# Kernel tuning notes

Measured on AMD Instinct MI355X. Metric: run time of the kernel, lower is better.

The kernel has to match this reference:

```python
import jax, jax.numpy as jnp
import numpy as np

B, S, D, H = 4, 2048, 512, 8
HD = D // H  # 64


def setup_inputs() -> dict:
    key = jax.random.key(0)
    ks = jax.random.split(key, 7)
    scale = 1.0 / np.sqrt(D)
    return {
        "query": jax.random.normal(ks[0], (B, S, D), jnp.float32),
        "key": jax.random.normal(ks[1], (B, S, D), jnp.float32),
        "value": jax.random.normal(ks[2], (B, S, D), jnp.float32),
        # Only the `query` Linear and fc_out are actually used in the original forward
        "Wq": jax.random.uniform(ks[3], (D, D), jnp.float32, -scale, scale),
        "bq": jnp.zeros((D,), jnp.float32),
        "Wo": jax.random.uniform(ks[4], (D, D), jnp.float32, -scale, scale),
        "bo": jnp.zeros((D,), jnp.float32),
    }


def reference(query, key, value, Wq, bq, Wo, bo):
    # Faithful to source: Q, K, V all use the *query* projection (bug preserved)
    def proj(x):
        # [B,S,D] -> [B,H,S,HD]
        y = x @ Wq + bq
        return y.reshape(B, S, H, HD).transpose(0, 2, 1, 3)

    Q, K, V = proj(query), proj(key), proj(value)
    scores = jnp.einsum("bhqd,bhkd->bhqk", Q, K) / jnp.sqrt(jnp.float32(HD))
    attn = jax.nn.softmax(scores, axis=-1)
    x = jnp.einsum("bhqk,bhkd->bhqd", attn, V)
    x = x.transpose(0, 2, 1, 3).reshape(B, S, D)
    return x @ Wo + bo
```

## Files before the change

kernel.cpp:

```cpp
#include <hip/hip_runtime.h>
#include <math.h>

#define B_ 4
#define S_ 2048
#define D_ 512
#define H_ 8
#define HD_ 64
#define SZ_ (B_ * S_ * D_)
#define WSZ_ (D_ * D_)
#define BSH_ (B_ * S_ * H_)

#define QSCALE_ 0.18033688011112042f

typedef _Float16 v4h __attribute__((ext_vector_type(4)));
typedef _Float16 v8h __attribute__((ext_vector_type(8)));
typedef float    v4f __attribute__((ext_vector_type(4)));

__device__ __forceinline__ void gload16(const void* g, void* l) {
    __builtin_amdgcn_global_load_lds((__attribute__((address_space(1))) void*)g,
                                     (__attribute__((address_space(3))) void*)l,
                                     16, 0, 0);
}

__device__ __forceinline__ v8h pack8(v4f a, v4f b) {
    return __builtin_shufflevector(__builtin_convertvector(a, v4h),
                                   __builtin_convertvector(b, v4h),
                                   0, 1, 2, 3, 4, 5, 6, 7);
}

__global__ __launch_bounds__(256) void wtrans_kernel(const float* __restrict__ Wq,
                                                     const float* __restrict__ Wo,
                                                     _Float16* __restrict__ Wt) {
    __shared__ float Ts[64][132];
    const int kc = blockIdx.x, nt = blockIdx.y, mat = blockIdx.z;
    const float* W = mat ? Wo : Wq;
    const int k0 = kc * 64, n0 = nt * 128;
    const int t = threadIdx.x;
#pragma unroll
    for (int i = 0; i < 8; i++) {
        int s2 = t + i * 256;
        int kk = s2 >> 5, nc = (s2 & 31) * 4;
        *(float4*)&Ts[kk][nc] = *(const float4*)&W[(size_t)(k0 + kk) * 512 + n0 + nc];
    }
    __syncthreads();
    _Float16* blk = Wt + (((size_t)mat * 4 + nt) * 8 + kc) * 8192;
#pragma unroll
    for (int i = 0; i < 4; i++) {
        int s2 = t + i * 256;
        int r = s2 >> 3, s = s2 & 7;
        int kl = (s ^ (r & 7)) * 8;
        v8h p;
#pragma unroll
        for (int j = 0; j < 8; j++) p[j] = (_Float16)Ts[kl + j][r];
        *(v8h*)&blk[r * 64 + s * 8] = p;
    }
}

__global__ __launch_bounds__(256) void convert_f16(const float* __restrict__ q,
                                                   const float* __restrict__ k,
                                                   const float* __restrict__ v,
                                                   _Float16* __restrict__ Xh) {
    const int kc = blockIdx.x, mt = blockIdx.y, z = blockIdx.z;
    const float* X = (z == 0) ? q : ((z == 1) ? k : v);
    _Float16* blk = Xh + (size_t)z * SZ_ + ((size_t)mt * 8 + kc) * 8192;
    const int t = threadIdx.x;
#pragma unroll
    for (int i = 0; i < 4; i++) {
        int s2 = t + i * 256;
        int r = s2 >> 3, s = s2 & 7;
        const float* src = X + (size_t)(mt * 128 + r) * 512 + kc * 64 + s * 8;
        *(v8h*)&blk[r * 64 + ((s ^ (r & 7)) * 8)] =
            pack8(*(const v4f*)src, *(const v4f*)(src + 4));
    }
}

__global__ __launch_bounds__(256) void combine_kernel(const float* __restrict__ Op,
                                                      const float* __restrict__ lp,
                                                      _Float16* __restrict__ Ah) {
    const int kc = blockIdx.x, mt = blockIdx.y;
    _Float16* blk = Ah + ((size_t)mt * 8 + kc) * 8192;
    const int t = threadIdx.x;
#pragma unroll
    for (int i = 0; i < 4; i++) {
        int s2 = t + i * 256;
        int r = s2 >> 3, s = s2 & 7;
        size_t row = (size_t)mt * 128 + r;
        const float* p = Op + row * 512 + kc * 64 + s * 8;
        const float* p2 = p + SZ_;
        float linv = __builtin_amdgcn_rcpf(lp[row * 8 + kc] + lp[BSH_ + row * 8 + kc]);
        v4f sa = (*(const v4f*)p + *(const v4f*)p2) * linv;
        v4f sb = (*(const v4f*)(p + 4) + *(const v4f*)(p2 + 4)) * linv;
        *(v8h*)&blk[r * 64 + ((s ^ (r & 7)) * 8)] = pack8(sa, sb);
    }
}

__global__ __launch_bounds__(256) void proj_mfma(const _Float16* __restrict__ Xh,
                                                 const _Float16* __restrict__ Wt,
                                                 const float* __restrict__ bq,
                                                 _Float16* __restrict__ Qh,
                                                 _Float16* __restrict__ Kh,
                                                 _Float16* __restrict__ VT) {
    __shared__ __align__(16) _Float16 As[8192];
    __shared__ __align__(16) _Float16 Bs[8192];
    const int nt = blockIdx.x, mt = blockIdx.y, z = blockIdx.z;
    const int n0 = nt * 128, m0 = mt * 128;
    const int t = threadIdx.x, lane = t & 63, w = t >> 6;
    const int wm = w >> 1, wn = w & 1;
    const int quad = lane >> 4, l16 = lane & 15;

    const _Float16* Ab = Xh + (size_t)z * SZ_ + ((size_t)mt * 8) * 8192 + w * 512 + lane * 8;
    const _Float16* Bb = Wt + ((size_t)nt * 8) * 8192 + w * 512 + lane * 8;
    _Float16* Ad = As + w * 512;
    _Float16* Bd = Bs + w * 512;

    v4f acc[4][4];
#pragma unroll
    for (int mi = 0; mi < 4; mi++)
#pragma unroll
        for (int ni = 0; ni < 4; ni++) acc[mi][ni] = (v4f)0.f;

    for (int kc = 0; kc < 8; ++kc) {
        __syncthreads();
#pragma unroll
        for (int i = 0; i < 4; i++) {
            gload16(Ab + kc * 8192 + i * 2048, Ad + i * 2048);
            gload16(Bb + kc * 8192 + i * 2048, Bd + i * 2048);
        }
        __syncthreads();

#pragma unroll
        for (int ks = 0; ks < 2; ++ks) {
            const int sxx = (ks * 32 + quad * 8) ^ ((l16 & 7) * 8);
            v8h af[4], bf[4];
#pragma unroll
            for (int mi = 0; mi < 4; mi++)
                af[mi] = *(const v8h*)&As[(wm * 64 + mi * 16 + l16) * 64 + sxx];
#pragma unroll
            for (int ni = 0; ni < 4; ni++)
                bf[ni] = *(const v8h*)&Bs[(wn * 64 + ni * 16 + l16) * 64 + sxx];
#pragma unroll
            for (int mi = 0; mi < 4; mi++)
#pragma unroll
                for (int ni = 0; ni < 4; ni++)
                    acc[mi][ni] = __builtin_amdgcn_mfma_f32_16x16x32_f16(af[mi], bf[ni], acc[mi][ni], 0, 0, 0);
        }
    }

    if (z < 2) {
        _Float16* Y = z ? Kh : Qh;
        const float sc = z ? 1.f : QSCALE_;
#pragma unroll
        for (int mi = 0; mi < 4; mi++) {
            int mb = m0 + wm * 64 + mi * 16 + quad * 4;
#pragma unroll
            for (int ni = 0; ni < 4; ni++) {
                int n = n0 + wn * 64 + ni * 16 + l16;
                float bj = bq[n];
#pragma unroll
                for (int r = 0; r < 4; r++)
                    Y[(size_t)(mb + r) * 512 + n] = (_Float16)((acc[mi][ni][r] + bj) * sc);
            }
        }
    } else {
#pragma unroll
        for (int mi = 0; mi < 4; mi++) {
            int tile0 = (m0 & 2047) + wm * 64;
            int pos = tile0 + (mi >> 1) * 32 + quad * 8 + (mi & 1) * 4;
            int b = m0 >> 11;
#pragma unroll
            for (int ni = 0; ni < 4; ni++) {
                int n = n0 + wn * 64 + ni * 16 + l16;
                int h = n >> 6, dd = n & 63;
                float bj = bq[n];
                v4h pk;
#pragma unroll
                for (int r = 0; r < 4; r++) pk[r] = (_Float16)(acc[mi][ni][r] + bj);
                *(v4h*)&VT[(((size_t)b * H_ + h) * HD_ + dd) * S_ + pos] = pk;
            }
        }
    }
}

__global__ __launch_bounds__(256) void outproj_mfma(const _Float16* __restrict__ Ah,
                                                    const _Float16* __restrict__ Wt,
                                                    const float* __restrict__ bo,
                                                    float* __restrict__ out) {
    __shared__ __align__(16) _Float16 As[8192];
    __shared__ __align__(16) _Float16 Bs[8192];
    const int nt = blockIdx.x, mt = blockIdx.y;
    const int n0 = nt * 128, m0 = mt * 128;
    const int t = threadIdx.x, lane = t & 63, w = t >> 6;
    const int wm = w >> 1, wn = w & 1;
    const int quad = lane >> 4, l16 = lane & 15;

    const _Float16* Ab = Ah + ((size_t)mt * 8) * 8192 + w * 512 + lane * 8;
    const _Float16* Bb = Wt + (size_t)(4 + nt) * 8 * 8192 + w * 512 + lane * 8;
    _Float16* Ad = As + w * 512;
    _Float16* Bd = Bs + w * 512;

    v4f acc[4][4];
#pragma unroll
    for (int mi = 0; mi < 4; mi++)
#pragma unroll
        for (int ni = 0; ni < 4; ni++) acc[mi][ni] = (v4f)0.f;

    for (int kc = 0; kc < 8; ++kc) {
        __syncthreads();
#pragma unroll
        for (int i = 0; i < 4; i++) {
            gload16(Ab + kc * 8192 + i * 2048, Ad + i * 2048);
            gload16(Bb + kc * 8192 + i * 2048, Bd + i * 2048);
        }
        __syncthreads();

#pragma unroll
        for (int ks = 0; ks < 2; ++ks) {
            const int sxx = (ks * 32 + quad * 8) ^ ((l16 & 7) * 8);
            v8h af[4], bf[4];
#pragma unroll
            for (int mi = 0; mi < 4; mi++)
                af[mi] = *(const v8h*)&As[(wm * 64 + mi * 16 + l16) * 64 + sxx];
#pragma unroll
            for (int ni = 0; ni < 4; ni++)
                bf[ni] = *(const v8h*)&Bs[(wn * 64 + ni * 16 + l16) * 64 + sxx];
#pragma unroll
            for (int mi = 0; mi < 4; mi++)
#pragma unroll
                for (int ni = 0; ni < 4; ni++)
                    acc[mi][ni] = __builtin_amdgcn_mfma_f32_16x16x32_f16(af[mi], bf[ni], acc[mi][ni], 0, 0, 0);
        }
    }

#pragma unroll
    for (int mi = 0; mi < 4; mi++) {
        int mb = m0 + wm * 64 + mi * 16 + quad * 4;
#pragma unroll
        for (int ni = 0; ni < 4; ni++) {
            int n = n0 + wn * 64 + ni * 16 + l16;
            float bj = bo[n];
#pragma unroll
            for (int r = 0; r < 4; r++)
                out[(size_t)(mb + r) * 512 + n] = acc[mi][ni][r] + bj;
        }
    }
}

__global__ __launch_bounds__(256) void flash_attn_f16(const _Float16* __restrict__ Qh,
                                                      const _Float16* __restrict__ Kh,
                                                      const _Float16* __restrict__ VT,
                                                      float* __restrict__ Op,
                                                      float* __restrict__ lp) {
    __shared__ _Float16 Ks[128 * 72];
    __shared__ _Float16 Vs[64 * 136];

    const int t     = threadIdx.x;
    const int lane  = t & 63;
    const int w     = t >> 6;
    const int quad  = lane >> 4;
    const int l16   = lane & 15;
    const int q0    = blockIdx.x * 128;
    const int h     = blockIdx.y;
    const int b     = blockIdx.z >> 1;
    const int split = blockIdx.z & 1;

    const size_t base  = (size_t)b * S_ * D_ + (size_t)h * HD_;
    const size_t vbase = ((size_t)b * H_ + h) * HD_ * (size_t)S_;

    v8h qf[2][2];
#pragma unroll
    for (int nb = 0; nb < 2; nb++) {
        const _Float16* qrow = Qh + base + (size_t)(q0 + w * 32 + nb * 16 + l16) * D_;
        qf[nb][0] = *(const v8h*)(qrow + quad * 8);
        qf[nb][1] = *(const v8h*)(qrow + 32 + quad * 8);
    }

    v4f o[2][4];
#pragma unroll
    for (int nb = 0; nb < 2; nb++)
#pragma unroll
        for (int i = 0; i < 4; i++) o[nb][i] = (v4f)0.f;
    float l_lane[2] = {0.f, 0.f};

    const int kbeg = split * (S_ / 2);
    const int kend = kbeg + S_ / 2;

    v8h kv[4], vv[4];
#define LOADKV(kk)                                                             \
    do {                                                                       \
        _Pragma("unroll") for (int i = 0; i < 4; i++) {                        \
            int c = t + i * 256;                                               \
            kv[i] = *(const v8h*)(Kh + base + (size_t)((kk) + (c >> 3)) * D_ + (c & 7) * 8); \
            vv[i] = *(const v8h*)(VT + vbase + (size_t)(c >> 4) * S_ + (kk) + (c & 15) * 8); \
        }                                                                      \
    } while (0)

    LOADKV(kbeg);

    for (int kk0 = kbeg; kk0 < kend; kk0 += 128) {
        __syncthreads();
#pragma unroll
        for (int i = 0; i < 4; i++) {
            int c = t + i * 256;
            *(v8h*)&Ks[(c >> 3) * 72 + (c & 7) * 8] = kv[i];
            *(v8h*)&Vs[(c >> 4) * 136 + (c & 15) * 8] = vv[i];
        }
        __syncthreads();

        if (kk0 + 128 < kend) LOADKV(kk0 + 128);

#pragma unroll
        for (int hh = 0; hh < 2; hh++) {
            v4f sc[4][2];
#pragma unroll
            for (int mb = 0; mb < 4; mb++)
#pragma unroll
                for (int nb = 0; nb < 2; nb++) sc[mb][nb] = (v4f)0.f;
#pragma unroll
            for (int ks = 0; ks < 2; ks++) {
#pragma unroll
                for (int mb = 0; mb < 4; mb++) {
                    v8h ak = *(const v8h*)&Ks[(hh * 64 + mb * 16 + l16) * 72 + ks * 32 + quad * 8];
#pragma unroll
                    for (int nb = 0; nb < 2; nb++)
                        sc[mb][nb] = __builtin_amdgcn_mfma_f32_16x16x32_f16(ak, qf[nb][ks], sc[mb][nb], 0, 0, 0);
                }
            }

            v4h pf[4][2];
#pragma unroll
            for (int nb = 0; nb < 2; nb++) {
#pragma unroll
                for (int mb = 0; mb < 4; mb++) {
                    v4f pv;
#pragma unroll
                    for (int r = 0; r < 4; r++) pv[r] = __builtin_amdgcn_exp2f(sc[mb][nb][r]);
                    pf[mb][nb] = __builtin_convertvector(pv, v4h);
                    l_lane[nb] += (pv[0] + pv[1]) + (pv[2] + pv[3]);
                }
            }

#pragma unroll
            for (int p = 0; p < 2; p++) {
#pragma unroll
                for (int dblk = 0; dblk < 4; dblk++) {
                    v8h vf2 = *(const v8h*)&Vs[(dblk * 16 + l16) * 136 + hh * 64 + p * 32 + quad * 8];
                    v4h vlo = __builtin_shufflevector(vf2, vf2, 0, 1, 2, 3);
                    v4h vhi = __builtin_shufflevector(vf2, vf2, 4, 5, 6, 7);
#pragma unroll
                    for (int nb = 0; nb < 2; nb++) {
                        o[nb][dblk] = __builtin_amdgcn_mfma_f32_16x16x16f16(vlo, pf[2 * p][nb], o[nb][dblk], 0, 0, 0);
                        o[nb][dblk] = __builtin_amdgcn_mfma_f32_16x16x16f16(vhi, pf[2 * p + 1][nb], o[nb][dblk], 0, 0, 0);
                    }
                }
            }
        }
    }
#undef LOADKV

    float* Ops = Op + (size_t)split * SZ_;
#pragma unroll
    for (int nb = 0; nb < 2; nb++) {
        float rs = l_lane[nb];
        rs += __shfl_xor(rs, 16);
        rs += __shfl_xor(rs, 32);
        int qrow = q0 + w * 32 + nb * 16 + l16;
        if (quad == 0)
            lp[(size_t)split * BSH_ + ((size_t)b * S_ + qrow) * H_ + h] = rs;
        const size_t rbase = base + (size_t)qrow * D_;
#pragma unroll
        for (int dblk = 0; dblk < 4; dblk++)
            *(v4f*)&Ops[rbase + dblk * 16 + quad * 4] = o[nb][dblk];
    }
}

extern "C" void kernel_launch(void* const* d_in, const int* in_sizes, int n_in,
                              void* d_out, int out_size, void* d_ws, size_t ws_size,
                              hipStream_t stream) {
    const float* query = (const float*)d_in[0];
    const float* key   = (const float*)d_in[1];
    const float* value = (const float*)d_in[2];
    const float* Wq    = (const float*)d_in[3];
    const float* bq    = (const float*)d_in[4];
    const float* Wo    = (const float*)d_in[5];
    const float* bo    = (const float*)d_in[6];
    float* out = (float*)d_out;

    _Float16* ws = (_Float16*)d_ws;
    _Float16* Qh = ws;
    _Float16* Kh = ws + (size_t)SZ_;
    _Float16* VT = ws + 2 * (size_t)SZ_;
    _Float16* Wt = ws + 3 * (size_t)SZ_;
    _Float16* Xh = ws + 3 * (size_t)SZ_ + 2 * (size_t)WSZ_;
    float*    Op = (float*)Xh;
    float*    lp = Op + 2 * (size_t)SZ_;
    _Float16* Ah = Qh;

    wtrans_kernel<<<dim3(8, 4, 2), 256, 0, stream>>>(Wq, Wo, Wt);
    convert_f16<<<dim3(8, 64, 3), 256, 0, stream>>>(query, key, value, Xh);
    proj_mfma<<<dim3(4, 64, 3), 256, 0, stream>>>(Xh, Wt, bq, Qh, Kh, VT);
    flash_attn_f16<<<dim3(S_ / 128, H_, B_ * 2), 256, 0, stream>>>(Qh, Kh, VT, Op, lp);
    combine_kernel<<<dim3(8, 64), 256, 0, stream>>>(Op, lp, Ah);
    outproj_mfma<<<dim3(4, 64), 256, 0, stream>>>(Ah, Wt, bo, out);
}
```

Before: 202.0 us.

## Drop KV split in attention, fuse normalization into epilogue, merge prep kernels

```diff
diff --git a/kernel.cpp b/kernel.cpp
--- a/kernel.cpp
+++ b/kernel.cpp
@@ -28,14 +28,33 @@
                                    0, 1, 2, 3, 4, 5, 6, 7);
 }
 
-__global__ __launch_bounds__(256) void wtrans_kernel(const float* __restrict__ Wq,
-                                                     const float* __restrict__ Wo,
-                                                     _Float16* __restrict__ Wt) {
+__global__ __launch_bounds__(256) void prep_f16(const float* __restrict__ q,
+                                                const float* __restrict__ k,
+                                                const float* __restrict__ v,
+                                                const float* __restrict__ Wq,
+                                                const float* __restrict__ Wo,
+                                                _Float16* __restrict__ Xh,
+                                                _Float16* __restrict__ Wt) {
+    const int kc = blockIdx.x, my = blockIdx.y, z = blockIdx.z;
+    const int t = threadIdx.x;
+    if (z < 3) {
+        const float* X = (z == 0) ? q : ((z == 1) ? k : v);
+        _Float16* blk = Xh + (size_t)z * SZ_ + ((size_t)my * 8 + kc) * 8192;
+#pragma unroll
+        for (int i = 0; i < 4; i++) {
+            int s2 = t + i * 256;
+            int r = s2 >> 3, s = s2 & 7;
+            const float* src = X + (size_t)(my * 128 + r) * 512 + kc * 64 + s * 8;
+            *(v8h*)&blk[r * 64 + ((s ^ (r & 7)) * 8)] =
+                pack8(*(const v4f*)src, *(const v4f*)(src + 4));
+        }
+        return;
+    }
+    if (my >= 8) return;
+    const int mat = my >> 2, nt = my & 3;
     __shared__ float Ts[64][132];
-    const int kc = blockIdx.x, nt = blockIdx.y, mat = blockIdx.z;
     const float* W = mat ? Wo : Wq;
     const int k0 = kc * 64, n0 = nt * 128;
-    const int t = threadIdx.x;
 #pragma unroll
     for (int i = 0; i < 8; i++) {
         int s2 = t + i * 256;
@@ -53,44 +72,6 @@
 #pragma unroll
         for (int j = 0; j < 8; j++) p[j] = (_Float16)Ts[kl + j][r];
         *(v8h*)&blk[r * 64 + s * 8] = p;
-    }
-}
-
-__global__ __launch_bounds__(256) void convert_f16(const float* __restrict__ q,
-                                                   const float* __restrict__ k,
-                                                   const float* __restrict__ v,
-                                                   _Float16* __restrict__ Xh) {
-    const int kc = blockIdx.x, mt = blockIdx.y, z = blockIdx.z;
-    const float* X = (z == 0) ? q : ((z == 1) ? k : v);
-    _Float16* blk = Xh + (size_t)z * SZ_ + ((size_t)mt * 8 + kc) * 8192;
-    const int t = threadIdx.x;
-#pragma unroll
-    for (int i = 0; i < 4; i++) {
-        int s2 = t + i * 256;
-        int r = s2 >> 3, s = s2 & 7;
-        const float* src = X + (size_t)(mt * 128 + r) * 512 + kc * 64 + s * 8;
-        *(v8h*)&blk[r * 64 + ((s ^ (r & 7)) * 8)] =
-            pack8(*(const v4f*)src, *(const v4f*)(src + 4));
-    }
-}
-
-__global__ __launch_bounds__(256) void combine_kernel(const float* __restrict__ Op,
-                                                      const float* __restrict__ lp,
-                                                      _Float16* __restrict__ Ah) {
-    const int kc = blockIdx.x, mt = blockIdx.y;
-    _Float16* blk = Ah + ((size_t)mt * 8 + kc) * 8192;
-    const int t = threadIdx.x;
-#pragma unroll
-    for (int i = 0; i < 4; i++) {
-        int s2 = t + i * 256;
-        int r = s2 >> 3, s = s2 & 7;
-        size_t row = (size_t)mt * 128 + r;
-        const float* p = Op + row * 512 + kc * 64 + s * 8;
-        const float* p2 = p + SZ_;
-        float linv = __builtin_amdgcn_rcpf(lp[row * 8 + kc] + lp[BSH_ + row * 8 + kc]);
-        v4f sa = (*(const v4f*)p + *(const v4f*)p2) * linv;
-        v4f sb = (*(const v4f*)(p + 4) + *(const v4f*)(p2 + 4)) * linv;
-        *(v8h*)&blk[r * 64 + ((s ^ (r & 7)) * 8)] = pack8(sa, sb);
     }
 }
 
@@ -248,8 +229,7 @@
 __global__ __launch_bounds__(256) void flash_attn_f16(const _Float16* __restrict__ Qh,
                                                       const _Float16* __restrict__ Kh,
                                                       const _Float16* __restrict__ VT,
-                                                      float* __restrict__ Op,
-                                                      float* __restrict__ lp) {
+                                                      _Float16* __restrict__ Ah) {
     __shared__ _Float16 Ks[128 * 72];
     __shared__ _Float16 Vs[64 * 136];
 
@@ -258,10 +238,12 @@
     const int w     = t >> 6;
     const int quad  = lane >> 4;
     const int l16   = lane & 15;
-    const int q0    = blockIdx.x * 128;
-    const int h     = blockIdx.y;
-    const int b     = blockIdx.z >> 1;
-    const int split = blockIdx.z & 1;
+    const int blk = blockIdx.x;
+    const int xcd = blk & 7, idx = blk >> 3;
+    const int pid = xcd * 4 + (idx >> 4);
+    const int qb  = idx & 15;
+    const int b   = pid >> 3, h = pid & 7;
+    const int q0  = qb * 128;
 
     const size_t base  = (size_t)b * S_ * D_ + (size_t)h * HD_;
     const size_t vbase = ((size_t)b * H_ + h) * HD_ * (size_t)S_;
@@ -280,9 +262,6 @@
 #pragma unroll
         for (int i = 0; i < 4; i++) o[nb][i] = (v4f)0.f;
     float l_lane[2] = {0.f, 0.f};
-
-    const int kbeg = split * (S_ / 2);
-    const int kend = kbeg + S_ / 2;
 
     v8h kv[4], vv[4];
 #define LOADKV(kk)                                                             \
@@ -294,9 +273,9 @@
         }                                                                      \
     } while (0)
 
-    LOADKV(kbeg);
-
-    for (int kk0 = kbeg; kk0 < kend; kk0 += 128) {
+    LOADKV(0);
+
+    for (int kk0 = 0; kk0 < S_; kk0 += 128) {
         __syncthreads();
 #pragma unroll
         for (int i = 0; i < 4; i++) {
@@ -306,7 +285,7 @@
         }
         __syncthreads();
 
-        if (kk0 + 128 < kend) LOADKV(kk0 + 128);
+        if (kk0 + 128 < S_) LOADKV(kk0 + 128);
 
 #pragma unroll
         for (int hh = 0; hh < 2; hh++) {
@@ -357,19 +336,22 @@
     }
 #undef LOADKV
 
-    float* Ops = Op + (size_t)split * SZ_;
 #pragma unroll
     for (int nb = 0; nb < 2; nb++) {
         float rs = l_lane[nb];
         rs += __shfl_xor(rs, 16);
         rs += __shfl_xor(rs, 32);
-        int qrow = q0 + w * 32 + nb * 16 + l16;
-        if (quad == 0)
-            lp[(size_t)split * BSH_ + ((size_t)b * S_ + qrow) * H_ + h] = rs;
-        const size_t rbase = base + (size_t)qrow * D_;
-#pragma unroll
-        for (int dblk = 0; dblk < 4; dblk++)
-            *(v4f*)&Ops[rbase + dblk * 16 + quad * 4] = o[nb][dblk];
+        float linv = __builtin_amdgcn_rcpf(rs);
+        int r = w * 32 + nb * 16 + l16;
+        _Float16* blkp = Ah + (((size_t)(b * 16 + qb)) * 8 + h) * 8192 + r * 64;
+#pragma unroll
+        for (int dblk = 0; dblk < 4; dblk++) {
+            int s = dblk * 2 + (quad >> 1);
+            v4h pk;
+#pragma unroll
+            for (int rr = 0; rr < 4; rr++) pk[rr] = (_Float16)(o[nb][dblk][rr] * linv);
+            *(v4h*)&blkp[((s ^ (r & 7)) * 8) + (quad & 1) * 4] = pk;
+        }
     }
 }
 
@@ -391,14 +373,10 @@
     _Float16* VT = ws + 2 * (size_t)SZ_;
     _Float16* Wt = ws + 3 * (size_t)SZ_;
     _Float16* Xh = ws + 3 * (size_t)SZ_ + 2 * (size_t)WSZ_;
-    float*    Op = (float*)Xh;
-    float*    lp = Op + 2 * (size_t)SZ_;
-    _Float16* Ah = Qh;
-
-    wtrans_kernel<<<dim3(8, 4, 2), 256, 0, stream>>>(Wq, Wo, Wt);
-    convert_f16<<<dim3(8, 64, 3), 256, 0, stream>>>(query, key, value, Xh);
+    _Float16* Ah = Xh;
+
+    prep_f16<<<dim3(8, 64, 4), 256, 0, stream>>>(query, key, value, Wq, Wo, Xh, Wt);
     proj_mfma<<<dim3(4, 64, 3), 256, 0, stream>>>(Xh, Wt, bq, Qh, Kh, VT);
-    flash_attn_f16<<<dim3(S_ / 128, H_, B_ * 2), 256, 0, stream>>>(Qh, Kh, VT, Op, lp);
-    combine_kernel<<<dim3(8, 64), 256, 0, stream>>>(Op, lp, Ah);
+    flash_attn_f16<<<dim3(512), 256, 0, stream>>>(Qh, Kh, VT, Ah);
     outproj_mfma<<<dim3(4, 64), 256, 0, stream>>>(Ah, Wt, bo, out);
 }
```

New measurement: 189.8 us. 6.0% less time.
